# Performance work log

Measured on AMD Instinct MI355X. Metric: run time of the kernel, lower is better.

The kernel has to match this reference:

```python
import jax, jax.numpy as jnp
import numpy as np

B, S, H, D = 2, 2048, 16, 64
HID = H * D
THETA = 10000.0
SCALING_FACTOR = 1
NEG_INF = -1e9


def _rope_cos_sin(position_ids):
    # Llama RoPE: inv_freq over even dims, duplicated halves.
    inv_freq = 1.0 / (THETA ** (jnp.arange(0, D, 2, dtype=jnp.float32) / D))  # [D/2]
    freqs = position_ids.astype(jnp.float32)[..., None] * inv_freq            # [B,S,D/2]
    emb = jnp.concatenate([freqs, freqs], axis=-1)                            # [B,S,D]
    return jnp.cos(emb), jnp.sin(emb)


def _rotate_half(x):
    x1, x2 = jnp.split(x, 2, axis=-1)
    return jnp.concatenate([-x2, x1], axis=-1)


def setup_inputs() -> dict:
    key = jax.random.key(0)
    ks = jax.random.split(key, 6)
    return {
        "hidden_states": jax.random.normal(ks[0], (B, S, HID), dtype=jnp.float32),
        "info_embeddings": jax.random.normal(ks[1], (B, S, HID), dtype=jnp.float32) * 0.1,
        "Wq": jax.random.normal(ks[2], (HID, HID), dtype=jnp.float32) * 0.02,
        "Wk": jax.random.normal(ks[3], (HID, HID), dtype=jnp.float32) * 0.02,
        "Wv": jax.random.normal(ks[4], (HID, HID), dtype=jnp.float32) * 0.02,
        "Wo": jax.random.normal(ks[5], (HID, HID), dtype=jnp.float32) * 0.02,
        "position_ids": jnp.broadcast_to(jnp.arange(S, dtype=jnp.int64), (B, S)),
    }


def reference(hidden_states, info_embeddings, Wq, Wk, Wv, Wo, position_ids):
    b, s, _ = hidden_states.shape
    # projections -> [B,H,S,D]
    q = (hidden_states @ Wq).reshape(b, s, H, D).transpose(0, 2, 1, 3)
    k = (hidden_states @ Wk).reshape(b, s, H, D).transpose(0, 2, 1, 3)
    v = (hidden_states @ Wv).reshape(b, s, H, D).transpose(0, 2, 1, 3)
    # info embedding added to q and k (pre-RoPE)
    info = info_embeddings.reshape(b, s, H, D).transpose(0, 2, 1, 3)
    q = q + info
    k = k + info
    # rotary position embedding
    cos, sin = _rope_cos_sin(position_ids)
    cos = cos[:, None]  # [B,1,S,D]
    sin = sin[:, None]
    q = q * cos + _rotate_half(q) * sin
    k = k * cos + _rotate_half(k) * sin
    # eager attention with custom scaling
    scale = 1.0 / float(np.sqrt(SCALING_FACTOR * D))
    scores = jnp.einsum("bhqd,bhkd->bhqk", q, k) * scale  # [B,H,S,S]
    causal = jnp.tril(jnp.ones((s, s), dtype=bool))
    scores = scores + jnp.where(causal, 0.0, NEG_INF).astype(scores.dtype)
    probs = jax.nn.softmax(scores, axis=-1)  # dropout p=0 (eval)
    attn = jnp.einsum("bhqk,bhkd->bhqd", probs, v)
    attn = attn.transpose(0, 2, 1, 3).reshape(b, s, HID)
    return attn @ Wo
```

## Files before the change

### kernel.cpp

```cpp
#include <hip/hip_runtime.h>
#include <hip/hip_bf16.h>

#define HB 2
#define HS 2048
#define HH 16
#define HD 64
#define HIDN 1024
#define MROWS 4096

typedef __attribute__((ext_vector_type(8))) short s16x8;
typedef __attribute__((ext_vector_type(4))) float f32x4;
typedef unsigned short u16;

__device__ inline u16 f2bf(float f) {
  union { __hip_bfloat16 h; u16 u; } cvt;
  cvt.h = __float2bfloat16(f);
  return cvt.u;
}

__device__ __forceinline__ void gload16(const u16* g, u16* l) {
  __builtin_amdgcn_global_load_lds((const __attribute__((address_space(1))) void*)g,
                                   (__attribute__((address_space(3))) void*)l, 16, 0, 0);
}

__global__ __launch_bounds__(256) void k_cvt(const float* __restrict__ in, u16* __restrict__ out, int n) {
  int i = (blockIdx.x * 256 + threadIdx.x) * 4;
  if (i >= n) return;
  float4 a = *(const float4*)(in + i);
  ushort4 r;
  r.x = f2bf(a.x); r.y = f2bf(a.y); r.z = f2bf(a.z); r.w = f2bf(a.w);
  *(ushort4*)(out + i) = r;
}

__global__ __launch_bounds__(256) void k_transpose(const float* __restrict__ W0, const float* __restrict__ W1,
                                                   const float* __restrict__ W2, const float* __restrict__ W3,
                                                   u16* __restrict__ out) {
  const float* W = (blockIdx.z == 0) ? W0 : (blockIdx.z == 1) ? W1 : (blockIdx.z == 2) ? W2 : W3;
  u16* O = out + (size_t)blockIdx.z * HIDN * HIDN;
  __shared__ float tile[64][65];
  int k0 = blockIdx.y * 64, c0 = blockIdx.x * 64;
  #pragma unroll
  for (int i = 0; i < 16; ++i) {
    int id = threadIdx.x + i * 256;
    int r = id >> 6, c = id & 63;
    tile[r][c] = W[(size_t)(k0 + r) * HIDN + c0 + c];
  }
  __syncthreads();
  #pragma unroll
  for (int i = 0; i < 16; ++i) {
    int id = threadIdx.x + i * 256;
    int r = id >> 6, c = id & 63;
    O[(size_t)(c0 + r) * HIDN + k0 + c] = f2bf(tile[c][r]);
  }
}

#define BM 128
#define BN 128
#define BK 64
#define LDK 72

__global__ __launch_bounds__(256) void k_qkv(const u16* __restrict__ X, const u16* __restrict__ Wt,
                                             const float* __restrict__ info,
                                             u16* __restrict__ Qb, u16* __restrict__ Kb, u16* __restrict__ Vt) {
  __shared__ __align__(16) u16 smem[128 * 136];
  const int bid = blockIdx.x;
  const int g   = bid & 7;
  const int idx = bid >> 3;
  const int nt  = idx & 7;
  const int ml  = (idx >> 3) & 3;
  const int z   = idx >> 5;
  const int mt  = g * 4 + ml;
  const u16* Bt = Wt + (size_t)z * HIDN * HIDN;
  const int tid = threadIdx.x;
  const int lane = tid & 63, wave = tid >> 6;
  const int wr = wave >> 1, wc = wave & 1;
  const int lg = lane >> 4, li = lane & 15;
  const int bm0 = mt * BM, bn0 = nt * BN;

  const int srow = lane >> 3;
  const int scol = (lane & 7) * 8;

  f32x4 acc[4][4];
  #pragma unroll
  for (int m = 0; m < 4; ++m)
    #pragma unroll
    for (int n = 0; n < 4; ++n) acc[m][n] = (f32x4){0.f, 0.f, 0.f, 0.f};

  for (int k0 = 0; k0 < HIDN; k0 += BK) {
    __syncthreads();
    #pragma unroll
    for (int c = 0; c < 4; ++c) {
      const int ci = wave * 4 + c;
      const int row = ci * 8 + srow;
      gload16(X  + (size_t)(bm0 + row) * HIDN + k0 + scol, &smem[ci * 512]);
      gload16(Bt + (size_t)(bn0 + row) * HIDN + k0 + scol, &smem[8192 + ci * 512]);
    }
    __syncthreads();
    #pragma unroll
    for (int kk = 0; kk < 2; ++kk) {
      s16x8 af[4], bfr[4];
      #pragma unroll
      for (int m = 0; m < 4; ++m) af[m]  = *(const s16x8*)(&smem[(wr * 64 + m * 16 + li) * 64 + kk * 32 + lg * 8]);
      #pragma unroll
      for (int n = 0; n < 4; ++n) bfr[n] = *(const s16x8*)(&smem[8192 + (wc * 64 + n * 16 + li) * 64 + kk * 32 + lg * 8]);
      __builtin_amdgcn_s_setprio(1);
      #pragma unroll
      for (int m = 0; m < 4; ++m)
        #pragma unroll
        for (int n = 0; n < 4; ++n)
          acc[m][n] = __builtin_amdgcn_mfma_f32_16x16x32_bf16(af[m], bfr[n], acc[m][n], 0, 0, 0);
      __builtin_amdgcn_s_setprio(0);
    }
  }

  if (z < 2) {
    u16* dst = (z == 0) ? Qb : Kb;
    #pragma unroll
    for (int m = 0; m < 4; ++m) {
      #pragma unroll
      for (int r = 0; r < 4; ++r) {
        int t = bm0 + wr * 64 + m * 16 + lg * 4 + r;
        int b = t >> 11, s = t & (HS - 1);
        #pragma unroll
        for (int n = 0; n < 2; ++n) {
          int c1 = bn0 + wc * 64 + n * 16 + li;
          float v1 = acc[m][n][r]     + info[(size_t)t * HIDN + c1];
          float v2 = acc[m][n + 2][r] + info[(size_t)t * HIDN + c1 + 32];
          int j = n * 16 + li;
          float invf = exp2f(-0.41524101186092030f * (float)j);
          float ang = (float)s * invf;
          float sn, cs;
          __sincosf(ang, &sn, &cs);
          float o1 = v1 * cs - v2 * sn;
          float o2 = v2 * cs + v1 * sn;
          if (z == 0) { o1 *= 0.18033688011f; o2 *= 0.18033688011f; }
          int h = c1 >> 6, d1 = c1 & 63;
          size_t base = ((size_t)(b * HH + h) * HS + s) * HD;
          dst[base + d1]      = f2bf(o1);
          dst[base + d1 + 32] = f2bf(o2);
        }
      }
    }
  } else {
    __syncthreads();
    #pragma unroll
    for (int m = 0; m < 4; ++m)
      #pragma unroll
      for (int n = 0; n < 4; ++n)
        #pragma unroll
        for (int r = 0; r < 4; ++r) {
          int cl = wc * 64 + n * 16 + li;
          int ml2 = wr * 64 + m * 16 + lg * 4 + r;
          smem[cl * 136 + ml2] = f2bf(acc[m][n][r]);
        }
    __syncthreads();
    const int b = bm0 >> 11, s0 = bm0 & (HS - 1);
    #pragma unroll
    for (int p = 0; p < 8; ++p) {
      int id = tid + p * 256;
      int cl = id >> 4, m8 = (id & 15) * 8;
      int c = bn0 + cl;
      int h = c >> 6, d = c & 63;
      s16x8 v = *(const s16x8*)(&smem[cl * 136 + m8]);
      *(s16x8*)(&Vt[((size_t)(b * HH + h) * HD + d) * HS + s0 + m8]) = v;
    }
  }
}

__global__ __launch_bounds__(256, 3) void k_attn(const u16* __restrict__ Qb, const u16* __restrict__ Kb,
                                                 const u16* __restrict__ Vt, u16* __restrict__ attnOut) {
  __shared__ u16 Ks[2][64 * LDK];
  __shared__ u16 Vs[2][64 * LDK];
  __shared__ u16 Ps[4][16 * LDK];
  const int bidx = blockIdx.x;
  const int bh = bidx & 31;
  const int j  = 31 - (bidx >> 5);
  const int q0 = j * 64;
  const int ntiles = j + 1;

  const u16* Qh = Qb + (size_t)bh * HS * HD;
  const u16* Kh = Kb + (size_t)bh * HS * HD;
  const u16* Vh = Vt + (size_t)bh * HD * HS;
  const int tid = threadIdx.x;
  const int lane = tid & 63, w = tid >> 6;
  const int lg = lane >> 4, li = lane & 15;
  const int b = bh >> 4, h = bh & 15;

  const int row16 = tid >> 3;
  const int col8  = (tid & 7) * 8;

  s16x8 qf[2];
  #pragma unroll
  for (int kk = 0; kk < 2; ++kk)
    qf[kk] = *(const s16x8*)(Qh + (size_t)(q0 + w * 16 + li) * HD + kk * 32 + lg * 8);

  f32x4 o[4];
  #pragma unroll
  for (int n = 0; n < 4; ++n) o[n] = (f32x4){0.f, 0.f, 0.f, 0.f};
  float lrow = 0.f;

  {
    uint4 ka = *(const uint4*)(Kh + (size_t)row16 * HD + col8);
    uint4 kb = *(const uint4*)(Kh + (size_t)(row16 + 32) * HD + col8);
    uint4 va = *(const uint4*)(Vh + (size_t)row16 * HS + col8);
    uint4 vb = *(const uint4*)(Vh + (size_t)(row16 + 32) * HS + col8);
    *(uint4*)(&Ks[0][row16 * LDK + col8])        = ka;
    *(uint4*)(&Ks[0][(row16 + 32) * LDK + col8]) = kb;
    *(uint4*)(&Vs[0][row16 * LDK + col8])        = va;
    *(uint4*)(&Vs[0][(row16 + 32) * LDK + col8]) = vb;
  }
  __syncthreads();

  for (int t = 0; t < ntiles; ++t) {
    const int cur = t & 1;
    uint4 rKa, rKb, rVa, rVb;
    const bool more = (t + 1 < ntiles);
    if (more) {
      const int kv1 = (t + 1) * 64;
      rKa = *(const uint4*)(Kh + (size_t)(kv1 + row16) * HD + col8);
      rKb = *(const uint4*)(Kh + (size_t)(kv1 + row16 + 32) * HD + col8);
      rVa = *(const uint4*)(Vh + (size_t)row16 * HS + kv1 + col8);
      rVb = *(const uint4*)(Vh + (size_t)(row16 + 32) * HS + kv1 + col8);
    }

    f32x4 sc[4];
    #pragma unroll
    for (int n = 0; n < 4; ++n) sc[n] = (f32x4){0.f, 0.f, 0.f, 0.f};
    __builtin_amdgcn_s_setprio(1);
    #pragma unroll
    for (int kk = 0; kk < 2; ++kk) {
      #pragma unroll
      for (int n = 0; n < 4; ++n) {
        s16x8 kfr = *(const s16x8*)(&Ks[cur][(n * 16 + li) * LDK + kk * 32 + lg * 8]);
        sc[n] = __builtin_amdgcn_mfma_f32_16x16x32_bf16(kfr, qf[kk], sc[n], 0, 0, 0);
      }
    }
    __builtin_amdgcn_s_setprio(0);

    if (t == ntiles - 1) {
      const int qrel = w * 16 + li;
      #pragma unroll
      for (int n = 0; n < 4; ++n)
        #pragma unroll
        for (int r = 0; r < 4; ++r)
          if (n * 16 + lg * 4 + r > qrel) sc[n][r] = -1e9f;
    }

    float psum = 0.f;
    #pragma unroll
    for (int n = 0; n < 4; ++n) {
      float p0 = exp2f(sc[n][0] - 8.0f);
      float p1 = exp2f(sc[n][1] - 8.0f);
      float p2 = exp2f(sc[n][2] - 8.0f);
      float p3 = exp2f(sc[n][3] - 8.0f);
      psum += (p0 + p1) + (p2 + p3);
      unsigned a0 = __float_as_uint(p0) + 0x8000u;
      unsigned a1 = __float_as_uint(p1) + 0x8000u;
      unsigned a2 = __float_as_uint(p2) + 0x8000u;
      unsigned a3 = __float_as_uint(p3) + 0x8000u;
      uint2 wv;
      wv.x = __builtin_amdgcn_perm(a1, a0, 0x07060302u);
      wv.y = __builtin_amdgcn_perm(a3, a2, 0x07060302u);
      *(uint2*)(&Ps[w][li * LDK + n * 16 + lg * 4]) = wv;
    }
    psum += __shfl_xor(psum, 16);
    psum += __shfl_xor(psum, 32);
    lrow += psum;

    __builtin_amdgcn_s_setprio(1);
    #pragma unroll
    for (int kk = 0; kk < 2; ++kk) {
      s16x8 pf = *(const s16x8*)(&Ps[w][li * LDK + kk * 32 + lg * 8]);
      #pragma unroll
      for (int n = 0; n < 4; ++n) {
        s16x8 vf = *(const s16x8*)(&Vs[cur][(n * 16 + li) * LDK + kk * 32 + lg * 8]);
        o[n] = __builtin_amdgcn_mfma_f32_16x16x32_bf16(pf, vf, o[n], 0, 0, 0);
      }
    }
    __builtin_amdgcn_s_setprio(0);

    if (more) {
      *(uint4*)(&Ks[cur ^ 1][row16 * LDK + col8])        = rKa;
      *(uint4*)(&Ks[cur ^ 1][(row16 + 32) * LDK + col8]) = rKb;
      *(uint4*)(&Vs[cur ^ 1][row16 * LDK + col8])        = rVa;
      *(uint4*)(&Vs[cur ^ 1][(row16 + 32) * LDK + col8]) = rVb;
      __syncthreads();
    }
  }

  float linv = 1.0f / lrow;
  float linvq[4];
  #pragma unroll
  for (int r = 0; r < 4; ++r) linvq[r] = __shfl(linv, lg * 4 + r);
  #pragma unroll
  for (int n = 0; n < 4; ++n)
    #pragma unroll
    for (int r = 0; r < 4; ++r) {
      int srow = q0 + w * 16 + lg * 4 + r;
      attnOut[(size_t)(b * HS + srow) * HIDN + h * 64 + n * 16 + li] = f2bf(o[n][r] * linvq[r]);
    }
}

__global__ __launch_bounds__(256) void k_out(const u16* __restrict__ A, const u16* __restrict__ Bt,
                                             float* __restrict__ out) {
  __shared__ __align__(16) u16 As[BM * 64];
  __shared__ __align__(16) u16 Bs[BN * 64];
  const int bid = blockIdx.x;
  const int g   = bid & 7;
  const int idx = bid >> 3;
  const int nt  = idx & 7;
  const int ml  = idx >> 3;
  const int mt  = g * 4 + ml;
  const int tid = threadIdx.x;
  const int lane = tid & 63, wave = tid >> 6;
  const int wr = wave >> 1, wc = wave & 1;
  const int lg = lane >> 4, li = lane & 15;
  const int bm0 = mt * BM, bn0 = nt * BN;

  const int srow = lane >> 3;
  const int scol = (lane & 7) * 8;

  f32x4 acc[4][4];
  #pragma unroll
  for (int m = 0; m < 4; ++m)
    #pragma unroll
    for (int n = 0; n < 4; ++n) acc[m][n] = (f32x4){0.f, 0.f, 0.f, 0.f};

  for (int k0 = 0; k0 < HIDN; k0 += BK) {
    __syncthreads();
    #pragma unroll
    for (int c = 0; c < 4; ++c) {
      const int ci = wave * 4 + c;
      const int row = ci * 8 + srow;
      gload16(A  + (size_t)(bm0 + row) * HIDN + k0 + scol, &As[ci * 512]);
      gload16(Bt + (size_t)(bn0 + row) * HIDN + k0 + scol, &Bs[ci * 512]);
    }
    __syncthreads();
    #pragma unroll
    for (int kk = 0; kk < 2; ++kk) {
      s16x8 af[4], bfr[4];
      #pragma unroll
      for (int m = 0; m < 4; ++m) af[m]  = *(const s16x8*)(&As[(wr * 64 + m * 16 + li) * 64 + kk * 32 + lg * 8]);
      #pragma unroll
      for (int n = 0; n < 4; ++n) bfr[n] = *(const s16x8*)(&Bs[(wc * 64 + n * 16 + li) * 64 + kk * 32 + lg * 8]);
      __builtin_amdgcn_s_setprio(1);
      #pragma unroll
      for (int m = 0; m < 4; ++m)
        #pragma unroll
        for (int n = 0; n < 4; ++n)
          acc[m][n] = __builtin_amdgcn_mfma_f32_16x16x32_bf16(af[m], bfr[n], acc[m][n], 0, 0, 0);
      __builtin_amdgcn_s_setprio(0);
    }
  }

  #pragma unroll
  for (int m = 0; m < 4; ++m)
    #pragma unroll
    for (int r = 0; r < 4; ++r) {
      int t = bm0 + wr * 64 + m * 16 + lg * 4 + r;
      #pragma unroll
      for (int n = 0; n < 4; ++n) {
        int c = bn0 + wc * 64 + n * 16 + li;
        out[(size_t)t * HIDN + c] = acc[m][n][r];
      }
    }
}

extern "C" void kernel_launch(void* const* d_in, const int* in_sizes, int n_in,
                              void* d_out, int out_size, void* d_ws, size_t ws_size,
                              hipStream_t stream) {
  const float* hs   = (const float*)d_in[0];
  const float* info = (const float*)d_in[1];
  const float* Wq   = (const float*)d_in[2];
  const float* Wk   = (const float*)d_in[3];
  const float* Wv   = (const float*)d_in[4];
  const float* Wo   = (const float*)d_in[5];
  float* out = (float*)d_out;

  char* ws = (char*)d_ws;
  u16* Xbf  = (u16*)(ws);
  u16* Wt   = (u16*)(ws + ((size_t)8  << 20));
  u16* Qb   = (u16*)(ws + ((size_t)16 << 20));
  u16* Kb   = (u16*)(ws + ((size_t)24 << 20));
  u16* Vt   = (u16*)(ws + ((size_t)32 << 20));
  u16* attn = Xbf;

  k_cvt<<<(MROWS * HIDN / 4 + 255) / 256, 256, 0, stream>>>(hs, Xbf, MROWS * HIDN);
  k_transpose<<<dim3(16, 16, 4), 256, 0, stream>>>(Wq, Wk, Wv, Wo, Wt);
  k_qkv<<<dim3(768), 256, 0, stream>>>(Xbf, Wt, info, Qb, Kb, Vt);
  k_attn<<<dim3(1024), 256, 0, stream>>>(Qb, Kb, Vt, attn);
  k_out<<<dim3(256), 256, 0, stream>>>(attn, Wt + (size_t)3 * HIDN * HIDN, out);
}
```

Baseline: 118.5 us.

## Process two query tiles per K/V pass and pair causal blocks per workgroup

The attention kernel now handles 128 query rows per pass, as two 64-row sub-tiles that share each loaded K/V tile, which halves K/V global and LDS traffic per query. Each workgroup runs two phases, a long block (15-p) and a short block (p), so causal work is balanced across 256 workgroups instead of launching 1024 uneven ones. The grid is now exactly one workgroup per CU on a 256-CU part, with fewer waves to hide latency. Register pressure roughly doubles, and the occupancy hint of 3 is dropped.

```diff
diff --git a/kernel.cpp b/kernel.cpp
--- a/kernel.cpp
+++ b/kernel.cpp
@@ -167,16 +167,14 @@
   }
 }
 
-__global__ __launch_bounds__(256, 3) void k_attn(const u16* __restrict__ Qb, const u16* __restrict__ Kb,
-                                                 const u16* __restrict__ Vt, u16* __restrict__ attnOut) {
+__global__ __launch_bounds__(256) void k_attn(const u16* __restrict__ Qb, const u16* __restrict__ Kb,
+                                              const u16* __restrict__ Vt, u16* __restrict__ attnOut) {
   __shared__ u16 Ks[2][64 * LDK];
   __shared__ u16 Vs[2][64 * LDK];
-  __shared__ u16 Ps[4][16 * LDK];
+  __shared__ u16 Ps[4][2][16 * LDK];
   const int bidx = blockIdx.x;
   const int bh = bidx & 31;
-  const int j  = 31 - (bidx >> 5);
-  const int q0 = j * 64;
-  const int ntiles = j + 1;
+  const int p  = bidx >> 5;
 
   const u16* Qh = Qb + (size_t)bh * HS * HD;
   const u16* Kh = Kb + (size_t)bh * HS * HD;
@@ -189,116 +187,181 @@
   const int row16 = tid >> 3;
   const int col8  = (tid & 7) * 8;
 
-  s16x8 qf[2];
-  #pragma unroll
-  for (int kk = 0; kk < 2; ++kk)
-    qf[kk] = *(const s16x8*)(Qh + (size_t)(q0 + w * 16 + li) * HD + kk * 32 + lg * 8);
-
-  f32x4 o[4];
-  #pragma unroll
-  for (int n = 0; n < 4; ++n) o[n] = (f32x4){0.f, 0.f, 0.f, 0.f};
-  float lrow = 0.f;
-
-  {
-    uint4 ka = *(const uint4*)(Kh + (size_t)row16 * HD + col8);
-    uint4 kb = *(const uint4*)(Kh + (size_t)(row16 + 32) * HD + col8);
-    uint4 va = *(const uint4*)(Vh + (size_t)row16 * HS + col8);
-    uint4 vb = *(const uint4*)(Vh + (size_t)(row16 + 32) * HS + col8);
-    *(uint4*)(&Ks[0][row16 * LDK + col8])        = ka;
-    *(uint4*)(&Ks[0][(row16 + 32) * LDK + col8]) = kb;
-    *(uint4*)(&Vs[0][row16 * LDK + col8])        = va;
-    *(uint4*)(&Vs[0][(row16 + 32) * LDK + col8]) = vb;
-  }
-  __syncthreads();
-
-  for (int t = 0; t < ntiles; ++t) {
-    const int cur = t & 1;
-    uint4 rKa, rKb, rVa, rVb;
-    const bool more = (t + 1 < ntiles);
-    if (more) {
-      const int kv1 = (t + 1) * 64;
-      rKa = *(const uint4*)(Kh + (size_t)(kv1 + row16) * HD + col8);
-      rKb = *(const uint4*)(Kh + (size_t)(kv1 + row16 + 32) * HD + col8);
-      rVa = *(const uint4*)(Vh + (size_t)row16 * HS + kv1 + col8);
-      rVb = *(const uint4*)(Vh + (size_t)(row16 + 32) * HS + kv1 + col8);
-    }
-
-    f32x4 sc[4];
-    #pragma unroll
-    for (int n = 0; n < 4; ++n) sc[n] = (f32x4){0.f, 0.f, 0.f, 0.f};
-    __builtin_amdgcn_s_setprio(1);
+  #pragma unroll
+  for (int ph = 0; ph < 2; ++ph) {
+    const int j  = ph ? p : 15 - p;
+    const int q0 = j * 128;
+    const int ntile = 2 * j + 2;
+
+    s16x8 qfA[2], qfB[2];
     #pragma unroll
     for (int kk = 0; kk < 2; ++kk) {
-      #pragma unroll
-      for (int n = 0; n < 4; ++n) {
-        s16x8 kfr = *(const s16x8*)(&Ks[cur][(n * 16 + li) * LDK + kk * 32 + lg * 8]);
-        sc[n] = __builtin_amdgcn_mfma_f32_16x16x32_bf16(kfr, qf[kk], sc[n], 0, 0, 0);
-      }
-    }
-    __builtin_amdgcn_s_setprio(0);
-
-    if (t == ntiles - 1) {
+      qfA[kk] = *(const s16x8*)(Qh + (size_t)(q0 + w * 16 + li) * HD + kk * 32 + lg * 8);
+      qfB[kk] = *(const s16x8*)(Qh + (size_t)(q0 + 64 + w * 16 + li) * HD + kk * 32 + lg * 8);
+    }
+
+    f32x4 oA[4], oB[4];
+    #pragma unroll
+    for (int n = 0; n < 4; ++n) { oA[n] = (f32x4){0.f,0.f,0.f,0.f}; oB[n] = (f32x4){0.f,0.f,0.f,0.f}; }
+    float lA = 0.f, lB = 0.f;
+
+    {
+      uint4 ka = *(const uint4*)(Kh + (size_t)row16 * HD + col8);
+      uint4 kb = *(const uint4*)(Kh + (size_t)(row16 + 32) * HD + col8);
+      uint4 va = *(const uint4*)(Vh + (size_t)row16 * HS + col8);
+      uint4 vb = *(const uint4*)(Vh + (size_t)(row16 + 32) * HS + col8);
+      __syncthreads();
+      *(uint4*)(&Ks[0][row16 * LDK + col8])        = ka;
+      *(uint4*)(&Ks[0][(row16 + 32) * LDK + col8]) = kb;
+      *(uint4*)(&Vs[0][row16 * LDK + col8])        = va;
+      *(uint4*)(&Vs[0][(row16 + 32) * LDK + col8]) = vb;
+    }
+    __syncthreads();
+
+    for (int t = 0; t < ntile; ++t) {
+      const int cur = t & 1;
+      const bool more = (t + 1 < ntile);
+      const bool doA  = (t <= 2 * j);
+      uint4 rKa, rKb, rVa, rVb;
+      if (more) {
+        const int kv1 = (t + 1) * 64;
+        rKa = *(const uint4*)(Kh + (size_t)(kv1 + row16) * HD + col8);
+        rKb = *(const uint4*)(Kh + (size_t)(kv1 + row16 + 32) * HD + col8);
+        rVa = *(const uint4*)(Vh + (size_t)row16 * HS + kv1 + col8);
+        rVb = *(const uint4*)(Vh + (size_t)(row16 + 32) * HS + kv1 + col8);
+      }
+
+      f32x4 scA[4], scB[4];
+      #pragma unroll
+      for (int n = 0; n < 4; ++n) { scA[n] = (f32x4){0.f,0.f,0.f,0.f}; scB[n] = (f32x4){0.f,0.f,0.f,0.f}; }
+      __builtin_amdgcn_s_setprio(1);
+      if (doA) {
+        #pragma unroll
+        for (int kk = 0; kk < 2; ++kk)
+          #pragma unroll
+          for (int n = 0; n < 4; ++n) {
+            s16x8 kfr = *(const s16x8*)(&Ks[cur][(n * 16 + li) * LDK + kk * 32 + lg * 8]);
+            scA[n] = __builtin_amdgcn_mfma_f32_16x16x32_bf16(kfr, qfA[kk], scA[n], 0, 0, 0);
+          }
+      }
+      #pragma unroll
+      for (int kk = 0; kk < 2; ++kk)
+        #pragma unroll
+        for (int n = 0; n < 4; ++n) {
+          s16x8 kfr = *(const s16x8*)(&Ks[cur][(n * 16 + li) * LDK + kk * 32 + lg * 8]);
+          scB[n] = __builtin_amdgcn_mfma_f32_16x16x32_bf16(kfr, qfB[kk], scB[n], 0, 0, 0);
+        }
+      __builtin_amdgcn_s_setprio(0);
+
       const int qrel = w * 16 + li;
-      #pragma unroll
-      for (int n = 0; n < 4; ++n)
-        #pragma unroll
-        for (int r = 0; r < 4; ++r)
-          if (n * 16 + lg * 4 + r > qrel) sc[n][r] = -1e9f;
-    }
-
-    float psum = 0.f;
-    #pragma unroll
-    for (int n = 0; n < 4; ++n) {
-      float p0 = exp2f(sc[n][0] - 8.0f);
-      float p1 = exp2f(sc[n][1] - 8.0f);
-      float p2 = exp2f(sc[n][2] - 8.0f);
-      float p3 = exp2f(sc[n][3] - 8.0f);
-      psum += (p0 + p1) + (p2 + p3);
-      unsigned a0 = __float_as_uint(p0) + 0x8000u;
-      unsigned a1 = __float_as_uint(p1) + 0x8000u;
-      unsigned a2 = __float_as_uint(p2) + 0x8000u;
-      unsigned a3 = __float_as_uint(p3) + 0x8000u;
-      uint2 wv;
-      wv.x = __builtin_amdgcn_perm(a1, a0, 0x07060302u);
-      wv.y = __builtin_amdgcn_perm(a3, a2, 0x07060302u);
-      *(uint2*)(&Ps[w][li * LDK + n * 16 + lg * 4]) = wv;
-    }
-    psum += __shfl_xor(psum, 16);
-    psum += __shfl_xor(psum, 32);
-    lrow += psum;
-
-    __builtin_amdgcn_s_setprio(1);
-    #pragma unroll
-    for (int kk = 0; kk < 2; ++kk) {
-      s16x8 pf = *(const s16x8*)(&Ps[w][li * LDK + kk * 32 + lg * 8]);
-      #pragma unroll
-      for (int n = 0; n < 4; ++n) {
-        s16x8 vf = *(const s16x8*)(&Vs[cur][(n * 16 + li) * LDK + kk * 32 + lg * 8]);
-        o[n] = __builtin_amdgcn_mfma_f32_16x16x32_bf16(pf, vf, o[n], 0, 0, 0);
-      }
-    }
-    __builtin_amdgcn_s_setprio(0);
-
-    if (more) {
-      *(uint4*)(&Ks[cur ^ 1][row16 * LDK + col8])        = rKa;
-      *(uint4*)(&Ks[cur ^ 1][(row16 + 32) * LDK + col8]) = rKb;
-      *(uint4*)(&Vs[cur ^ 1][row16 * LDK + col8])        = rVa;
-      *(uint4*)(&Vs[cur ^ 1][(row16 + 32) * LDK + col8]) = rVb;
-      __syncthreads();
-    }
-  }
-
-  float linv = 1.0f / lrow;
-  float linvq[4];
-  #pragma unroll
-  for (int r = 0; r < 4; ++r) linvq[r] = __shfl(linv, lg * 4 + r);
-  #pragma unroll
-  for (int n = 0; n < 4; ++n)
-    #pragma unroll
-    for (int r = 0; r < 4; ++r) {
-      int srow = q0 + w * 16 + lg * 4 + r;
-      attnOut[(size_t)(b * HS + srow) * HIDN + h * 64 + n * 16 + li] = f2bf(o[n][r] * linvq[r]);
-    }
+      if (t == 2 * j) {
+        #pragma unroll
+        for (int n = 0; n < 4; ++n)
+          #pragma unroll
+          for (int r = 0; r < 4; ++r)
+            if (n * 16 + lg * 4 + r > qrel) scA[n][r] = -1e9f;
+      }
+      if (t == 2 * j + 1) {
+        #pragma unroll
+        for (int n = 0; n < 4; ++n)
+          #pragma unroll
+          for (int r = 0; r < 4; ++r)
+            if (n * 16 + lg * 4 + r > qrel) scB[n][r] = -1e9f;
+      }
+
+      if (doA) {
+        float psum = 0.f;
+        #pragma unroll
+        for (int n = 0; n < 4; ++n) {
+          float p0 = exp2f(scA[n][0] - 8.0f);
+          float p1 = exp2f(scA[n][1] - 8.0f);
+          float p2 = exp2f(scA[n][2] - 8.0f);
+          float p3 = exp2f(scA[n][3] - 8.0f);
+          psum += (p0 + p1) + (p2 + p3);
+          unsigned a0 = __float_as_uint(p0) + 0x8000u;
+          unsigned a1 = __float_as_uint(p1) + 0x8000u;
+          unsigned a2 = __float_as_uint(p2) + 0x8000u;
+          unsigned a3 = __float_as_uint(p3) + 0x8000u;
+          uint2 wv;
+          wv.x = __builtin_amdgcn_perm(a1, a0, 0x07060302u);
+          wv.y = __builtin_amdgcn_perm(a3, a2, 0x07060302u);
+          *(uint2*)(&Ps[w][0][li * LDK + n * 16 + lg * 4]) = wv;
+        }
+        psum += __shfl_xor(psum, 16);
+        psum += __shfl_xor(psum, 32);
+        lA += psum;
+
+        __builtin_amdgcn_s_setprio(1);
+        #pragma unroll
+        for (int kk = 0; kk < 2; ++kk) {
+          s16x8 pf = *(const s16x8*)(&Ps[w][0][li * LDK + kk * 32 + lg * 8]);
+          #pragma unroll
+          for (int n = 0; n < 4; ++n) {
+            s16x8 vf = *(const s16x8*)(&Vs[cur][(n * 16 + li) * LDK + kk * 32 + lg * 8]);
+            oA[n] = __builtin_amdgcn_mfma_f32_16x16x32_bf16(pf, vf, oA[n], 0, 0, 0);
+          }
+        }
+        __builtin_amdgcn_s_setprio(0);
+      }
+
+      {
+        float psum = 0.f;
+        #pragma unroll
+        for (int n = 0; n < 4; ++n) {
+          float p0 = exp2f(scB[n][0] - 8.0f);
+          float p1 = exp2f(scB[n][1] - 8.0f);
+          float p2 = exp2f(scB[n][2] - 8.0f);
+          float p3 = exp2f(scB[n][3] - 8.0f);
+          psum += (p0 + p1) + (p2 + p3);
+          unsigned a0 = __float_as_uint(p0) + 0x8000u;
+          unsigned a1 = __float_as_uint(p1) + 0x8000u;
+          unsigned a2 = __float_as_uint(p2) + 0x8000u;
+          unsigned a3 = __float_as_uint(p3) + 0x8000u;
+          uint2 wv;
+          wv.x = __builtin_amdgcn_perm(a1, a0, 0x07060302u);
+          wv.y = __builtin_amdgcn_perm(a3, a2, 0x07060302u);
+          *(uint2*)(&Ps[w][1][li * LDK + n * 16 + lg * 4]) = wv;
+        }
+        psum += __shfl_xor(psum, 16);
+        psum += __shfl_xor(psum, 32);
+        lB += psum;
+
+        __builtin_amdgcn_s_setprio(1);
+        #pragma unroll
+        for (int kk = 0; kk < 2; ++kk) {
+          s16x8 pf = *(const s16x8*)(&Ps[w][1][li * LDK + kk * 32 + lg * 8]);
+          #pragma unroll
+          for (int n = 0; n < 4; ++n) {
+            s16x8 vf = *(const s16x8*)(&Vs[cur][(n * 16 + li) * LDK + kk * 32 + lg * 8]);
+            oB[n] = __builtin_amdgcn_mfma_f32_16x16x32_bf16(pf, vf, oB[n], 0, 0, 0);
+          }
+        }
+        __builtin_amdgcn_s_setprio(0);
+      }
+
+      if (more) {
+        *(uint4*)(&Ks[cur ^ 1][row16 * LDK + col8])        = rKa;
+        *(uint4*)(&Ks[cur ^ 1][(row16 + 32) * LDK + col8]) = rKb;
+        *(uint4*)(&Vs[cur ^ 1][row16 * LDK + col8])        = rVa;
+        *(uint4*)(&Vs[cur ^ 1][(row16 + 32) * LDK + col8]) = rVb;
+        __syncthreads();
+      }
+    }
+
+    float linvA = 1.0f / lA, linvB = 1.0f / lB;
+    float lqA[4], lqB[4];
+    #pragma unroll
+    for (int r = 0; r < 4; ++r) { lqA[r] = __shfl(linvA, lg * 4 + r); lqB[r] = __shfl(linvB, lg * 4 + r); }
+    #pragma unroll
+    for (int n = 0; n < 4; ++n)
+      #pragma unroll
+      for (int r = 0; r < 4; ++r) {
+        int srowA = q0 + w * 16 + lg * 4 + r;
+        int srowB = srowA + 64;
+        attnOut[(size_t)(b * HS + srowA) * HIDN + h * 64 + n * 16 + li] = f2bf(oA[n][r] * lqA[r]);
+        attnOut[(size_t)(b * HS + srowB) * HIDN + h * 64 + n * 16 + li] = f2bf(oB[n][r] * lqB[r]);
+      }
+  }
 }
 
 __global__ __launch_bounds__(256) void k_out(const u16* __restrict__ A, const u16* __restrict__ Bt,
@@ -388,6 +451,6 @@
   k_cvt<<<(MROWS * HIDN / 4 + 255) / 256, 256, 0, stream>>>(hs, Xbf, MROWS * HIDN);
   k_transpose<<<dim3(16, 16, 4), 256, 0, stream>>>(Wq, Wk, Wv, Wo, Wt);
   k_qkv<<<dim3(768), 256, 0, stream>>>(Xbf, Wt, info, Qb, Kb, Vt);
-  k_attn<<<dim3(1024), 256, 0, stream>>>(Qb, Kb, Vt, attn);
+  k_attn<<<dim3(256), 256, 0, stream>>>(Qb, Kb, Vt, attn);
   k_out<<<dim3(256), 256, 0, stream>>>(attn, Wt + (size_t)3 * HIDN * HIDN, out);
 }
```

New measurement: 138.7 us. 1.17x slower.
